# Optimization experiments

Hardware: AMD Instinct MI355X
Metric: run time of the kernel (lower is better)

The kernel has to match this reference:

```python
import jax, jax.numpy as jnp
import numpy as np

B, S, D, H = 2, 2048, 1024, 16
DK = D // H


def setup_inputs() -> dict:
    key = jax.random.key(0)
    ks = jax.random.split(key, 12)
    scale = 1.0 / np.sqrt(D)
    inp = {
        "q": jax.random.normal(ks[0], (B, S, D), dtype=jnp.float32),
        "k": jax.random.normal(ks[1], (B, S, D), dtype=jnp.float32),
        "v": jax.random.normal(ks[2], (B, S, D), dtype=jnp.float32),
        "mask": jax.random.randint(ks[3], (B, 1, 1, S), 0, 2, dtype=jnp.int32),
        "Wq": jax.random.normal(ks[4], (D, D), dtype=jnp.float32) * scale,
        "bq": jnp.zeros((D,), dtype=jnp.float32),
        "Wk": jax.random.normal(ks[5], (D, D), dtype=jnp.float32) * scale,
        "bk": jnp.zeros((D,), dtype=jnp.float32),
        "Wv": jax.random.normal(ks[6], (D, D), dtype=jnp.float32) * scale,
        "bv": jnp.zeros((D,), dtype=jnp.float32),
        "Wo": jax.random.normal(ks[7], (D, D), dtype=jnp.float32) * scale,
        "bo": jnp.zeros((D,), dtype=jnp.float32),
    }
    return inp


def reference(q, k, v, mask, Wq, bq, Wk, bk, Wv, bv, Wo, bo):
    # Linear projections (torch nn.Linear: x @ W.T + b)
    query = q @ Wq.T + bq                      # [B,S,D]
    key = k @ Wk.T + bk
    value = v @ Wv.T + bv
    # split heads -> [B,H,S,DK]
    def split(x):
        return x.reshape(B, S, H, DK).transpose(0, 2, 1, 3)
    qh, kh, vh = split(query), split(key), split(value)
    # scaled dot-product attention with additive mask
    scores = jnp.einsum("bhqd,bhkd->bhqk", qh, kh) / jnp.sqrt(jnp.float32(DK))
    scores = jnp.where(mask == 0, jnp.float32(-1e9), scores)
    attn = jax.nn.softmax(scores, axis=-1)     # [B,H,S,S]
    out = jnp.einsum("bhqk,bhkd->bhqd", attn, vh)
    out = out.transpose(0, 2, 1, 3).reshape(B, S, D)
    return out @ Wo.T + bo
```

## Files before the change

kernel.cpp:

```cpp
#include <hip/hip_runtime.h>


constexpr int BB = 2;
constexpr int SS = 2048;
constexpr int DD = 1024;
constexpr int HH = 16;
constexpr int DKK = 64;

typedef float f32x4 __attribute__((ext_vector_type(4)));
typedef __bf16 bf16x8 __attribute__((ext_vector_type(8)));
typedef short s16x8 __attribute__((ext_vector_type(8)));
typedef short s16x4 __attribute__((ext_vector_type(4)));

#define DEV static __device__ __forceinline__

DEV f32x4 mfma16(s16x8 a, s16x8 b, f32x4 c) {
  return __builtin_amdgcn_mfma_f32_16x16x32_bf16(
      __builtin_bit_cast(bf16x8, a), __builtin_bit_cast(bf16x8, b), c, 0, 0, 0);
}

DEV void split1(float x, short& h, short& l) {
  unsigned u = __float_as_uint(x);
  h = (short)(u >> 16);
  float hf = __uint_as_float(u & 0xffff0000u);
  l = (short)(__float_as_uint(x - hf) >> 16);
}
DEV short f2bf_rne(float x) {
  unsigned u = __float_as_uint(x);
  return (short)((u + 0x7fffu + ((u >> 16) & 1u)) >> 16);
}
DEV unsigned cvtpk(float lo, float hi) {
  unsigned r;
  asm("v_cvt_pk_bf16_f32 %0, %1, %2" : "=v"(r) : "v"(lo), "v"(hi));
  return r;
}
DEV s16x8 load8s(const short* p) { return *(const s16x8*)p; }

DEV void gld_lds16(const short* g, short* l) {
  __builtin_amdgcn_global_load_lds(
      (const __attribute__((address_space(1))) void*)g,
      (__attribute__((address_space(3))) void*)l, 16, 0, 0);
}

DEV void split4(const float* __restrict__ X, short* __restrict__ H,
                short* __restrict__ L, int i) {
  float4 x = *(const float4*)(X + i);
  float xs[4] = {x.x, x.y, x.z, x.w};
  s16x4 h4, l4;
#pragma unroll
  for (int e = 0; e < 4; ++e) {
    short h, l;
    split1(xs[e], h, l);
    h4[e] = h;
    l4[e] = l;
  }
  *(s16x4*)(H + i) = h4;
  *(s16x4*)(L + i) = l4;
}

DEV void cast4(const float* __restrict__ X, short* __restrict__ Y, int i) {
  float4 x = *(const float4*)(X + i);
  float xs[4] = {x.x, x.y, x.z, x.w};
  s16x4 y4;
#pragma unroll
  for (int e = 0; e < 4; ++e) y4[e] = f2bf_rne(xs[e]);
  *(s16x4*)(Y + i) = y4;
}

__global__ __launch_bounds__(256) void prep(
    const float* __restrict__ Wq, short* __restrict__ Wqh, short* __restrict__ Wql,
    const float* __restrict__ Wk, short* __restrict__ Wkh, short* __restrict__ Wkl,
    const float* __restrict__ Wo, short* __restrict__ Woh, short* __restrict__ Wol,
    const float* __restrict__ Wv, short* __restrict__ Wvh,
    const float* __restrict__ q, short* __restrict__ qH, short* __restrict__ qL,
    const float* __restrict__ k, short* __restrict__ kH, short* __restrict__ kL) {
  const int bid = blockIdx.x;
  const int t = threadIdx.x;
  if (bid < 4096) {
    const int w = bid >> 10;
    const int i = ((bid & 1023) * 256 + t) * 4;
    if (w == 0) split4(Wq, Wqh, Wql, i);
    else if (w == 1) split4(Wk, Wkh, Wkl, i);
    else if (w == 2) split4(Wo, Woh, Wol, i);
    else cast4(Wv, Wvh, i);
  } else {
    const int a = (bid - 4096) >> 12;
    const int i = (((bid - 4096) & 4095) * 256 + t) * 4;
    if (a == 0) split4(q, qH, qL, i);
    else split4(k, kH, kL, i);
  }
}

__global__ __launch_bounds__(256) void cast_rne(const float* __restrict__ X,
                                                short* __restrict__ Y) {
  int i = (blockIdx.x * 256 + threadIdx.x) * 4;
  cast4(X, Y, i);
}

__global__ __launch_bounds__(256) void gemm_qk(
    const short* __restrict__ qAh, const short* __restrict__ qAl,
    const short* __restrict__ Wqh, const short* __restrict__ Wql,
    const float* __restrict__ bq, short* __restrict__ Qo,
    const short* __restrict__ kAh, const short* __restrict__ kAl,
    const short* __restrict__ Wkh, const short* __restrict__ Wkl,
    const float* __restrict__ bk, short* __restrict__ Kho,
    short* __restrict__ Klo) {
  __shared__ short lds[2][12288];

  const int tid = threadIdx.x;
  const int lane = tid & 63, wv = tid >> 6;
  const int lo16 = lane & 15, quad = lane >> 4;
  const int sel = blockIdx.x >> 9;
  const int bid = blockIdx.x & 511;
  const int m0 = (bid & 31) * 128;
  const int n0 = (bid >> 5) * 64;

  const short* Agh = sel ? kAh : qAh;
  const short* Agl = sel ? kAl : qAl;
  const short* Wgh = sel ? Wkh : Wqh;
  const short* Wgl = sel ? Wkl : Wql;
  const float* bias = sel ? bk : bq;

  f32x4 acc[2][4];
#pragma unroll
  for (int mt = 0; mt < 2; ++mt)
#pragma unroll
    for (int nt = 0; nt < 4; ++nt) acc[mt][nt] = f32x4{0.f, 0.f, 0.f, 0.f};

  const int rw = tid >> 2, qw = tid & 3;
  const int ra0 = tid >> 2, ra1 = (tid + 256) >> 2;

  auto stage = [&](int k0, int buf) {
    short* sAh = lds[buf];
    short* sAl = lds[buf] + 4096;
    short* sWh = lds[buf] + 8192;
    short* sWl = lds[buf] + 10240;
    gld_lds16(Wgh + (size_t)(n0 + rw) * DD + k0 + qw * 8, sWh + tid * 8);
    gld_lds16(Wgl + (size_t)(n0 + rw) * DD + k0 + qw * 8, sWl + tid * 8);
    gld_lds16(Agh + (size_t)(m0 + ra0) * DD + k0 + qw * 8, sAh + tid * 8);
    gld_lds16(Agh + (size_t)(m0 + ra1) * DD + k0 + qw * 8, sAh + (tid + 256) * 8);
    gld_lds16(Agl + (size_t)(m0 + ra0) * DD + k0 + qw * 8, sAl + tid * 8);
    gld_lds16(Agl + (size_t)(m0 + ra1) * DD + k0 + qw * 8, sAl + (tid + 256) * 8);
  };

  stage(0, 0);

  for (int kk = 0; kk < DD / 32; ++kk) {
    __syncthreads();
    if (kk + 1 < DD / 32) stage((kk + 1) * 32, (kk + 1) & 1);

    const short* sAh = lds[kk & 1];
    const short* sAl = lds[kk & 1] + 4096;
    const short* sWh = lds[kk & 1] + 8192;
    const short* sWl = lds[kk & 1] + 10240;

    s16x8 ah[2], al[2], wh[4], wl[4];
#pragma unroll
    for (int mt = 0; mt < 2; ++mt) {
      const int r = wv * 32 + mt * 16 + lo16;
      ah[mt] = *(const s16x8*)&sAh[r * 32 + quad * 8];
      al[mt] = *(const s16x8*)&sAl[r * 32 + quad * 8];
    }
#pragma unroll
    for (int nt = 0; nt < 4; ++nt) {
      const int r = nt * 16 + lo16;
      wh[nt] = *(const s16x8*)&sWh[r * 32 + quad * 8];
      wl[nt] = *(const s16x8*)&sWl[r * 32 + quad * 8];
    }
#pragma unroll
    for (int mt = 0; mt < 2; ++mt)
#pragma unroll
      for (int nt = 0; nt < 4; ++nt) {
        acc[mt][nt] = mfma16(ah[mt], wh[nt], acc[mt][nt]);
        acc[mt][nt] = mfma16(ah[mt], wl[nt], acc[mt][nt]);
        acc[mt][nt] = mfma16(al[mt], wh[nt], acc[mt][nt]);
      }
  }

#pragma unroll
  for (int mt = 0; mt < 2; ++mt)
#pragma unroll
    for (int nt = 0; nt < 4; ++nt) {
      const int n = n0 + nt * 16 + lo16;
      const float bv = bias[n];
#pragma unroll
      for (int r = 0; r < 4; ++r) {
        const int m = m0 + wv * 32 + mt * 16 + quad * 4 + r;
        const float val = acc[mt][nt][r] + bv;
        const int b = m >> 11, s = m & 2047;
        const int h = n >> 6, dk = n & 63;
        if (sel == 0) {
          size_t idx = ((size_t)(b * HH + h) * SS + s) * DKK + dk;
          Qo[idx] = f2bf_rne(val);
        } else {
          const int dk_sw = dk ^ ((s & 7) << 3);
          size_t idx = ((size_t)(b * HH + h) * SS + s) * DKK + dk_sw;
          short hh, ll;
          split1(val, hh, ll);
          Kho[idx] = hh;
          Klo[idx] = ll;
        }
      }
    }
}

template <int SPLIT, int EPI>
__global__ __launch_bounds__(256) void gemm_tile(
    const short* __restrict__ Agh, const short* __restrict__ Agl,
    const short* __restrict__ Wgh, const short* __restrict__ Wgl,
    const float* __restrict__ bias, void* __restrict__ O1, void* __restrict__ O2) {
  __shared__ short lds[2][12288];

  const int tid = threadIdx.x;
  const int lane = tid & 63, wv = tid >> 6;
  const int lo16 = lane & 15, quad = lane >> 4;
  const int m0 = (blockIdx.x & 31) * 128;
  const int n0 = (blockIdx.x >> 5) * 64;

  f32x4 acc[2][4];
#pragma unroll
  for (int mt = 0; mt < 2; ++mt)
#pragma unroll
    for (int nt = 0; nt < 4; ++nt) acc[mt][nt] = f32x4{0.f, 0.f, 0.f, 0.f};

  const int rw = tid >> 2, qw = tid & 3;
  const int ra0 = tid >> 2, ra1 = (tid + 256) >> 2;

  auto stage = [&](int k0, int buf) {
    short* sAh = lds[buf];
    short* sAl = lds[buf] + 4096;
    short* sWh = lds[buf] + 8192;
    short* sWl = lds[buf] + 10240;
    gld_lds16(Wgh + (size_t)(n0 + rw) * DD + k0 + qw * 8, sWh + tid * 8);
    if constexpr (SPLIT)
      gld_lds16(Wgl + (size_t)(n0 + rw) * DD + k0 + qw * 8, sWl + tid * 8);
    gld_lds16(Agh + (size_t)(m0 + ra0) * DD + k0 + qw * 8, sAh + tid * 8);
    gld_lds16(Agh + (size_t)(m0 + ra1) * DD + k0 + qw * 8, sAh + (tid + 256) * 8);
    if constexpr (SPLIT) {
      gld_lds16(Agl + (size_t)(m0 + ra0) * DD + k0 + qw * 8, sAl + tid * 8);
      gld_lds16(Agl + (size_t)(m0 + ra1) * DD + k0 + qw * 8, sAl + (tid + 256) * 8);
    }
  };

  stage(0, 0);

  for (int kk = 0; kk < DD / 32; ++kk) {
    __syncthreads();
    if (kk + 1 < DD / 32) stage((kk + 1) * 32, (kk + 1) & 1);

    const short* sAh = lds[kk & 1];
    const short* sAl = lds[kk & 1] + 4096;
    const short* sWh = lds[kk & 1] + 8192;
    const short* sWl = lds[kk & 1] + 10240;

    s16x8 ah[2], al[2], wh[4], wl[4];
#pragma unroll
    for (int mt = 0; mt < 2; ++mt) {
      const int r = wv * 32 + mt * 16 + lo16;
      ah[mt] = *(const s16x8*)&sAh[r * 32 + quad * 8];
      if constexpr (SPLIT) al[mt] = *(const s16x8*)&sAl[r * 32 + quad * 8];
    }
#pragma unroll
    for (int nt = 0; nt < 4; ++nt) {
      const int r = nt * 16 + lo16;
      wh[nt] = *(const s16x8*)&sWh[r * 32 + quad * 8];
      if constexpr (SPLIT) wl[nt] = *(const s16x8*)&sWl[r * 32 + quad * 8];
    }
#pragma unroll
    for (int mt = 0; mt < 2; ++mt)
#pragma unroll
      for (int nt = 0; nt < 4; ++nt) {
        acc[mt][nt] = mfma16(ah[mt], wh[nt], acc[mt][nt]);
        if constexpr (SPLIT) {
          acc[mt][nt] = mfma16(ah[mt], wl[nt], acc[mt][nt]);
          acc[mt][nt] = mfma16(al[mt], wh[nt], acc[mt][nt]);
        }
      }
  }

#pragma unroll
  for (int mt = 0; mt < 2; ++mt)
#pragma unroll
    for (int nt = 0; nt < 4; ++nt) {
      const int n = n0 + nt * 16 + lo16;
      const float bv = bias[n];
#pragma unroll
      for (int r = 0; r < 4; ++r) {
        const int m = m0 + wv * 32 + mt * 16 + quad * 4 + r;
        const float val = acc[mt][nt][r] + bv;
        const int b = m >> 11, s = m & 2047;
        const int h = n >> 6, dk = n & 63;
        if constexpr (EPI == 1) {
          const int s_sw = s ^ ((dk & 7) << 3);
          size_t idx = ((size_t)(b * HH + h) * DKK + dk) * SS + s_sw;
          ((short*)O1)[idx] = f2bf_rne(val);
        } else {
          ((float*)O1)[(size_t)m * DD + n] = val;
        }
      }
    }
}

constexpr int PAD = 68;
constexpr int NKB = SS / 64;
constexpr float EXPSC = 0.125f * 1.4426950408889634f;

__global__ __launch_bounds__(256, 2) void mha_attn(
    const short* __restrict__ Qh, const short* __restrict__ Kh,
    const short* __restrict__ Kl, const short* __restrict__ Vt,
    const int* __restrict__ mask, short* __restrict__ Ah,
    short* __restrict__ Al) {
  __shared__ short sKV[2][12288];
  __shared__ short sP[4][32 * PAD];

  const int tid = threadIdx.x;
  const int lane = tid & 63, wv = tid >> 6;
  const int lo16 = lane & 15, quad = lane >> 4;
  const int bid = blockIdx.x;
  const int head = (bid & 7) * 4 + ((bid >> 3) & 3);
  const int qblk = bid >> 5;
  const int q0 = qblk * 128 + wv * 32;
  const int b = head >> 4;

  const size_t hbase = (size_t)head * SS;
  const size_t vbase = (size_t)head * DKK;

  constexpr short ONE_BF = (short)0x3F80;
  const s16x8 ones8 = {ONE_BF, ONE_BF, ONE_BF, ONE_BF,
                       ONE_BF, ONE_BF, ONE_BF, ONE_BF};

  s16x8 qh[2][2];
#pragma unroll
  for (int rt = 0; rt < 2; ++rt) {
    size_t qb = (hbase + q0 + rt * 16 + lo16) * DKK + quad * 8;
#pragma unroll
    for (int c = 0; c < 2; ++c) qh[rt][c] = load8s(Qh + qb + c * 32);
  }

  f32x4 Oacc[2][4];
#pragma unroll
  for (int rt = 0; rt < 2; ++rt)
#pragma unroll
    for (int t = 0; t < 4; ++t) Oacc[rt][t] = f32x4{0.f, 0.f, 0.f, 0.f};
  f32x4 sacc[2];
  sacc[0] = f32x4{0.f, 0.f, 0.f, 0.f};
  sacc[1] = f32x4{0.f, 0.f, 0.f, 0.f};

  auto STAGE = [&](int k0, int buf) {
    short* base = &sKV[buf][0];
#pragma unroll
    for (int i = 0; i < 2; ++i) {
      const int ch = tid + 256 * i;
      const int row = ch >> 3;
      const int inner = (ch & 7) * 8;
      gld_lds16(Kh + (hbase + k0 + row) * DKK + inner, base + ch * 8);
      gld_lds16(Kl + (hbase + k0 + row) * DKK + inner, base + 4096 + ch * 8);
      gld_lds16(Vt + (vbase + row) * SS + k0 + inner, base + 8192 + ch * 8);
    }
  };

  STAGE(0, 0);

  for (int kb = 0; kb < NKB; ++kb) {
    const int k0g = kb * 64;
    const int cur = kb & 1;
    __syncthreads();

    if (kb + 1 < NKB) STAGE(k0g + 64, cur ^ 1);

    const short* sKh = &sKV[cur][0];
    const short* sKl = &sKV[cur][4096];
    const short* sV = &sKV[cur][8192];

    float addf[4][4];
#pragma unroll
    for (int sub = 0; sub < 4; ++sub) {
      const int4 mq = *(const int4*)(mask + b * SS + k0g + sub * 16 + quad * 4);
      addf[sub][0] = mq.x ? 0.f : -32768.f;
      addf[sub][1] = mq.y ? 0.f : -32768.f;
      addf[sub][2] = mq.z ? 0.f : -32768.f;
      addf[sub][3] = mq.w ? 0.f : -32768.f;
    }

    f32x4 sc4[2][4];
    __builtin_amdgcn_s_setprio(1);
#pragma unroll
    for (int sub = 0; sub < 4; ++sub) {
      sc4[0][sub] = f32x4{0.f, 0.f, 0.f, 0.f};
      sc4[1][sub] = f32x4{0.f, 0.f, 0.f, 0.f};
      const int krow = sub * 16 + lo16;
      const int ksw = (krow & 7) << 3;
#pragma unroll
      for (int c = 0; c < 2; ++c) {
        const int koff = krow * 64 + ((c * 32 + quad * 8) ^ ksw);
        s16x8 kh = *(const s16x8*)&sKh[koff];
        s16x8 kl = *(const s16x8*)&sKl[koff];
#pragma unroll
        for (int rt = 0; rt < 2; ++rt) {
          sc4[rt][sub] = mfma16(kh, qh[rt][c], sc4[rt][sub]);
          sc4[rt][sub] = mfma16(kl, qh[rt][c], sc4[rt][sub]);
        }
      }
    }
    __builtin_amdgcn_s_setprio(0);

#pragma unroll
    for (int rt = 0; rt < 2; ++rt) {
      const int prow = (rt * 16 + lo16) * PAD;
#pragma unroll
      for (int sub = 0; sub < 4; ++sub) {
        const float p0 = exp2f(fmaf(sc4[rt][sub][0], EXPSC, addf[sub][0]));
        const float p1 = exp2f(fmaf(sc4[rt][sub][1], EXPSC, addf[sub][1]));
        const float p2 = exp2f(fmaf(sc4[rt][sub][2], EXPSC, addf[sub][2]));
        const float p3 = exp2f(fmaf(sc4[rt][sub][3], EXPSC, addf[sub][3]));
        *(unsigned*)&sP[wv][prow + sub * 16 + quad * 4] = cvtpk(p0, p1);
        *(unsigned*)&sP[wv][prow + sub * 16 + quad * 4 + 2] = cvtpk(p2, p3);
      }
    }

    s16x8 pa[2][2];
#pragma unroll
    for (int rt = 0; rt < 2; ++rt)
#pragma unroll
      for (int c = 0; c < 2; ++c)
        pa[rt][c] = *(const s16x8*)&sP[wv][(rt * 16 + lo16) * PAD + c * 32 + quad * 8];
    __builtin_amdgcn_s_setprio(1);
#pragma unroll
    for (int rt = 0; rt < 2; ++rt) {
      sacc[rt] = mfma16(pa[rt][0], ones8, sacc[rt]);
      sacc[rt] = mfma16(pa[rt][1], ones8, sacc[rt]);
    }
#pragma unroll
    for (int t = 0; t < 4; ++t) {
      const int vrow = t * 16 + lo16;
      const int vsw = (vrow & 7) << 3;
#pragma unroll
      for (int c = 0; c < 2; ++c) {
        s16x8 vb = *(const s16x8*)&sV[vrow * 64 + ((c * 32 + quad * 8) ^ vsw)];
#pragma unroll
        for (int rt = 0; rt < 2; ++rt)
          Oacc[rt][t] = mfma16(pa[rt][c], vb, Oacc[rt][t]);
      }
    }
    __builtin_amdgcn_s_setprio(0);
  }

  const int h = head & 15;
#pragma unroll
  for (int rt = 0; rt < 2; ++rt) {
#pragma unroll
    for (int r = 0; r < 4; ++r) {
      const float rinv = 1.0f / sacc[rt][r];
#pragma unroll
      for (int t = 0; t < 4; ++t) {
        const float val = Oacc[rt][t][r] * rinv;
        const int row = q0 + rt * 16 + quad * 4 + r;
        const int col = h * DKK + t * 16 + lo16;
        const size_t idx = ((size_t)b * SS + row) * DD + col;
        short hh, ll;
        split1(val, hh, ll);
        Ah[idx] = hh;
        Al[idx] = ll;
      }
    }
  }
}

extern "C" void kernel_launch(void* const* d_in, const int* in_sizes, int n_in,
                              void* d_out, int out_size, void* d_ws, size_t ws_size,
                              hipStream_t stream) {
  const float* q = (const float*)d_in[0];
  const float* k = (const float*)d_in[1];
  const float* v = (const float*)d_in[2];
  const int* mask = (const int*)d_in[3];
  const float* Wq = (const float*)d_in[4];
  const float* bq = (const float*)d_in[5];
  const float* Wk = (const float*)d_in[6];
  const float* bk = (const float*)d_in[7];
  const float* Wv = (const float*)d_in[8];
  const float* bv = (const float*)d_in[9];
  const float* Wo = (const float*)d_in[10];
  const float* bo = (const float*)d_in[11];

  char* ws = (char*)d_ws;
  size_t off = 0;
  auto take = [&](size_t bytes) {
    char* p = ws + off;
    off += (bytes + 255) & ~(size_t)255;
    return p;
  };
  const size_t WE = (size_t)DD * DD;
  const size_t TE = (size_t)BB * SS * DD;

  short* Wqh = (short*)take(WE * 2);
  short* Wql = (short*)take(WE * 2);
  short* Wkh = (short*)take(WE * 2);
  short* Wkl = (short*)take(WE * 2);
  short* Wvh = (short*)take(WE * 2);
  short* Woh = (short*)take(WE * 2);
  short* Wol = (short*)take(WE * 2);
  short* qH = (short*)take(TE * 2);
  short* qL = (short*)take(TE * 2);
  short* kH = (short*)take(TE * 2);
  short* kL = (short*)take(TE * 2);
  short* Qh = (short*)take(TE * 2);
  short* Kh = (short*)take(TE * 2);
  short* Kl = (short*)take(TE * 2);
  (void)ws_size;
  short* vH = qH;
  short* Vt = qL;
  short* aH = kH;
  short* aL = kL;

  prep<<<12288, 256, 0, stream>>>(Wq, Wqh, Wql, Wk, Wkh, Wkl, Wo, Woh, Wol,
                                  Wv, Wvh, q, qH, qL, k, kH, kL);

  gemm_qk<<<1024, 256, 0, stream>>>(qH, qL, Wqh, Wql, bq, Qh,
                                    kH, kL, Wkh, Wkl, bk, Kh, Kl);

  cast_rne<<<4096, 256, 0, stream>>>(v, vH);
  gemm_tile<0, 1><<<512, 256, 0, stream>>>(vH, nullptr, Wvh, nullptr, bv, Vt, nullptr);

  mha_attn<<<512, 256, 0, stream>>>(Qh, Kh, Kl, Vt, mask, aH, aL);

  gemm_tile<1, 2><<<512, 256, 0, stream>>>(aH, aL, Woh, Wol, bo, d_out, nullptr);
}
```

Baseline: 312.6 us.

## Keep softmax probabilities in registers using transposed 16x16x16 MFMA, vectorize output stores

The probability tile no longer round-trips through shared memory. The attention is computed in transposed form with the 16x16x16 bf16 MFMA, so the exp outputs feed the P·V and row-sum MFMAs directly as B operands. The V-transpose swizzle in the projection epilogue changes to match the new 4-element LDS reads. The output epilogue goes through a per-wave LDS transpose so it can write 4-wide vectorized hi/lo stores instead of scalar ones. The trade-off is twice as many (smaller) MFMA instructions, plus an inline-asm fallback with conservative nops.

```diff
diff --git a/kernel.cpp b/kernel.cpp
--- a/kernel.cpp
+++ b/kernel.cpp
@@ -11,6 +11,7 @@
 typedef __bf16 bf16x8 __attribute__((ext_vector_type(8)));
 typedef short s16x8 __attribute__((ext_vector_type(8)));
 typedef short s16x4 __attribute__((ext_vector_type(4)));
+typedef unsigned u32x2 __attribute__((ext_vector_type(2)));
 
 #define DEV static __device__ __forceinline__
 
@@ -18,6 +19,23 @@
   return __builtin_amdgcn_mfma_f32_16x16x32_bf16(
       __builtin_bit_cast(bf16x8, a), __builtin_bit_cast(bf16x8, b), c, 0, 0, 0);
 }
+
+#if __has_builtin(__builtin_amdgcn_mfma_f32_16x16x16bf16_1k)
+DEV f32x4 mfma16k(s16x4 a, s16x4 b, f32x4 c) {
+  return __builtin_amdgcn_mfma_f32_16x16x16bf16_1k(a, b, c, 0, 0, 0);
+}
+#else
+DEV f32x4 mfma16k(s16x4 a, s16x4 b, f32x4 c) {
+  asm volatile(
+      "s_nop 1\n\t"
+      "v_mfma_f32_16x16x16_bf16 %0, %1, %2, %0\n\t"
+      "s_nop 7\n\t"
+      "s_nop 7"
+      : "+v"(c)
+      : "v"(a), "v"(b));
+  return c;
+}
+#endif
 
 DEV void split1(float x, short& h, short& l) {
   unsigned u = __float_as_uint(x);
@@ -291,7 +309,7 @@
         const int b = m >> 11, s = m & 2047;
         const int h = n >> 6, dk = n & 63;
         if constexpr (EPI == 1) {
-          const int s_sw = s ^ ((dk & 7) << 3);
+          const int s_sw = s ^ ((dk & 3) << 4);
           size_t idx = ((size_t)(b * HH + h) * DKK + dk) * SS + s_sw;
           ((short*)O1)[idx] = f2bf_rne(val);
         } else {
@@ -301,7 +319,6 @@
     }
 }
 
-constexpr int PAD = 68;
 constexpr int NKB = SS / 64;
 constexpr float EXPSC = 0.125f * 1.4426950408889634f;
 
@@ -310,8 +327,7 @@
     const short* __restrict__ Kl, const short* __restrict__ Vt,
     const int* __restrict__ mask, short* __restrict__ Ah,
     short* __restrict__ Al) {
-  __shared__ short sKV[2][12288];
-  __shared__ short sP[4][32 * PAD];
+  __shared__ __align__(16) short sKV[2][12288];
 
   const int tid = threadIdx.x;
   const int lane = tid & 63, wv = tid >> 6;
@@ -326,8 +342,7 @@
   const size_t vbase = (size_t)head * DKK;
 
   constexpr short ONE_BF = (short)0x3F80;
-  const s16x8 ones8 = {ONE_BF, ONE_BF, ONE_BF, ONE_BF,
-                       ONE_BF, ONE_BF, ONE_BF, ONE_BF};
+  const s16x4 ones4 = {ONE_BF, ONE_BF, ONE_BF, ONE_BF};
 
   s16x8 qh[2][2];
 #pragma unroll
@@ -404,64 +419,71 @@
     }
     __builtin_amdgcn_s_setprio(0);
 
-#pragma unroll
-    for (int rt = 0; rt < 2; ++rt) {
-      const int prow = (rt * 16 + lo16) * PAD;
+    s16x4 pb[2][4];
+#pragma unroll
+    for (int rt = 0; rt < 2; ++rt)
 #pragma unroll
       for (int sub = 0; sub < 4; ++sub) {
         const float p0 = exp2f(fmaf(sc4[rt][sub][0], EXPSC, addf[sub][0]));
         const float p1 = exp2f(fmaf(sc4[rt][sub][1], EXPSC, addf[sub][1]));
         const float p2 = exp2f(fmaf(sc4[rt][sub][2], EXPSC, addf[sub][2]));
         const float p3 = exp2f(fmaf(sc4[rt][sub][3], EXPSC, addf[sub][3]));
-        *(unsigned*)&sP[wv][prow + sub * 16 + quad * 4] = cvtpk(p0, p1);
-        *(unsigned*)&sP[wv][prow + sub * 16 + quad * 4 + 2] = cvtpk(p2, p3);
-      }
-    }
-
-    s16x8 pa[2][2];
+        u32x2 w;
+        w[0] = cvtpk(p0, p1);
+        w[1] = cvtpk(p2, p3);
+        pb[rt][sub] = __builtin_bit_cast(s16x4, w);
+      }
+
+    __builtin_amdgcn_s_setprio(1);
 #pragma unroll
     for (int rt = 0; rt < 2; ++rt)
 #pragma unroll
-      for (int c = 0; c < 2; ++c)
-        pa[rt][c] = *(const s16x8*)&sP[wv][(rt * 16 + lo16) * PAD + c * 32 + quad * 8];
-    __builtin_amdgcn_s_setprio(1);
-#pragma unroll
-    for (int rt = 0; rt < 2; ++rt) {
-      sacc[rt] = mfma16(pa[rt][0], ones8, sacc[rt]);
-      sacc[rt] = mfma16(pa[rt][1], ones8, sacc[rt]);
-    }
+      for (int sub = 0; sub < 4; ++sub)
+        sacc[rt] = mfma16k(ones4, pb[rt][sub], sacc[rt]);
 #pragma unroll
     for (int t = 0; t < 4; ++t) {
       const int vrow = t * 16 + lo16;
-      const int vsw = (vrow & 7) << 3;
-#pragma unroll
-      for (int c = 0; c < 2; ++c) {
-        s16x8 vb = *(const s16x8*)&sV[vrow * 64 + ((c * 32 + quad * 8) ^ vsw)];
+      const int vsw = (lo16 & 3) << 4;
+#pragma unroll
+      for (int sub = 0; sub < 4; ++sub) {
+        s16x4 va = *(const s16x4*)&sV[vrow * 64 + ((sub * 16 + quad * 4) ^ vsw)];
 #pragma unroll
         for (int rt = 0; rt < 2; ++rt)
-          Oacc[rt][t] = mfma16(pa[rt][c], vb, Oacc[rt][t]);
+          Oacc[rt][t] = mfma16k(va, pb[rt][sub], Oacc[rt][t]);
       }
     }
     __builtin_amdgcn_s_setprio(0);
   }
 
+  __syncthreads();
+  float* sT = (float*)&sKV[0][0] + wv * (16 * 68);
   const int h = head & 15;
 #pragma unroll
   for (int rt = 0; rt < 2; ++rt) {
-#pragma unroll
-    for (int r = 0; r < 4; ++r) {
-      const float rinv = 1.0f / sacc[rt][r];
-#pragma unroll
-      for (int t = 0; t < 4; ++t) {
-        const float val = Oacc[rt][t][r] * rinv;
-        const int row = q0 + rt * 16 + quad * 4 + r;
-        const int col = h * DKK + t * 16 + lo16;
-        const size_t idx = ((size_t)b * SS + row) * DD + col;
-        short hh, ll;
-        split1(val, hh, ll);
-        Ah[idx] = hh;
-        Al[idx] = ll;
-      }
+    const float rinv = 1.0f / sacc[rt][0];
+#pragma unroll
+    for (int t = 0; t < 4; ++t) {
+      f32x4 vv;
+#pragma unroll
+      for (int r = 0; r < 4; ++r) vv[r] = Oacc[rt][t][r] * rinv;
+      *(f32x4*)&sT[lo16 * 68 + t * 16 + quad * 4] = vv;
+    }
+#pragma unroll
+    for (int i = 0; i < 4; ++i) {
+      const int qrow = quad + 4 * i;
+      f32x4 vv = *(const f32x4*)&sT[qrow * 68 + lo16 * 4];
+      const int row = q0 + rt * 16 + qrow;
+      const size_t idx = ((size_t)b * SS + row) * DD + h * DKK + lo16 * 4;
+      s16x4 hh, ll;
+#pragma unroll
+      for (int e = 0; e < 4; ++e) {
+        short he, le;
+        split1(vv[e], he, le);
+        hh[e] = he;
+        ll[e] = le;
+      }
+      *(s16x4*)&Ah[idx] = hh;
+      *(s16x4*)&Al[idx] = ll;
     }
   }
 }
```

Result: no change. 315.8 us (+1.0%).
